# Kernel tuning notes

Measured on AMD Instinct MI355X. Metric: run time of the kernel, lower is better.

Reference implementation:

```python
import jax, jax.numpy as jnp
import numpy as np

EMBED_DIM = 512
NUM_HEADS = 8
TGT_LEN = 1024
BSZ = 16


def setup_inputs() -> dict:
    key = jax.random.key(0)
    ks = jax.random.split(key, 6)
    E = EMBED_DIM
    query = jax.random.normal(ks[0], (TGT_LEN, BSZ, E), jnp.float32)
    i_proj = jax.random.normal(ks[1], (3 * E,), jnp.float32)
    # xavier_uniform-ish scale for (3E, E)
    lim = (6.0 / (3 * E + E)) ** 0.5
    in_proj_weight = jax.random.uniform(ks[2], (3 * E, E), jnp.float32, -lim, lim)
    in_proj_bias = jnp.zeros((3 * E,), jnp.float32)
    lim2 = (6.0 / (2 * E)) ** 0.5
    out_w = jax.random.uniform(ks[3], (E, E), jnp.float32, -lim2, lim2)
    out_b = jnp.zeros((E,), jnp.float32)
    bias_k = jax.random.normal(ks[4], (1, 1, E), jnp.float32)
    bias_v = jax.random.normal(ks[5], (1, 1, E), jnp.float32)
    return dict(query=query, i_proj=i_proj, in_proj_weight=in_proj_weight,
                in_proj_bias=in_proj_bias, out_w=out_w, out_b=out_b,
                bias_k=bias_k, bias_v=bias_v)


def reference(query, i_proj, in_proj_weight, in_proj_bias, out_w, out_b, bias_k, bias_v):
    # qkv_same path: key = value = query (self-attention)
    T, B, E = query.shape
    H = NUM_HEADS
    hd = E // H
    scaling = hd ** -0.5
    # per-call weight mutation: every 3rd column replaced by i_proj
    w = in_proj_weight.at[:, ::3].set(i_proj[:, None])
    qkv = jnp.einsum('tbe,fe->tbf', query, w) + in_proj_bias  # (T, B, 3E)
    q, k, v = jnp.split(qkv, 3, axis=-1)
    q = q * scaling
    k = jnp.concatenate([k, jnp.broadcast_to(bias_k, (1, B, E))], axis=0)  # (T+1, B, E)
    v = jnp.concatenate([v, jnp.broadcast_to(bias_v, (1, B, E))], axis=0)
    S = k.shape[0]
    q = q.reshape(T, B * H, hd).transpose(1, 0, 2)  # (B*H, T, hd)
    k = k.reshape(S, B * H, hd).transpose(1, 0, 2)  # (B*H, S, hd)
    v = v.reshape(S, B * H, hd).transpose(1, 0, 2)
    aw = jnp.einsum('nth,nsh->nts', q, k)  # (B*H, T, S)
    # global min-max normalization over the entire score tensor (not softmax)
    mn = jnp.min(aw)
    mx = jnp.max(aw)
    aw = (aw - mn) / (mx - mn)
    attn = jnp.einsum('nts,nsh->nth', aw, v)  # (B*H, T, hd)
    attn = attn.transpose(1, 0, 2).reshape(T, B, E)
    attn = attn @ out_w.T + out_b  # out_proj
    aw_avg = aw.reshape(B, H, T, S).sum(axis=1) / H  # (B, T, S)
    wq, wk, wv = jnp.split(w, 3, axis=0)
    w_ret = jnp.stack([wq.T, wk.T, wv.T], axis=0)  # (3, E, E)
    return attn, aw_avg, w_ret
```

## Files before the change

### kernel.cpp

```cpp
#include <hip/hip_runtime.h>
#include <hip/hip_bf16.h>
#include <stdint.h>

typedef __bf16 bf16;
typedef __bf16 bf16x8 __attribute__((ext_vector_type(8)));
typedef __bf16 bf16x4 __attribute__((ext_vector_type(4)));
typedef float  f32x4  __attribute__((ext_vector_type(4)));

#define MFMA_BF16(a,b,c) __builtin_amdgcn_mfma_f32_16x16x32_bf16((a),(b),(c),0,0,0)

#define WS_QBF_IN  0L
#define WS_WBF     16777216L
#define WS_OUTWBF  18350080L
#define WS_Q       18874368L
#define WS_K       35651584L
#define WS_V       52428800L
#define WS_VT      69206016L
#define WS_AWLAST  85983232L
#define WS_VCS     86507520L
#define WS_MM      86540288L
#define WS_KT      86540544L
#define WS_KTV     103317760L

__device__ __forceinline__ void gload16(const void* g, void* l) {
  __builtin_amdgcn_global_load_lds((const __attribute__((address_space(1))) uint32_t*)g,
                                   (__attribute__((address_space(3))) uint32_t*)l, 16, 0, 0);
}
__device__ __forceinline__ unsigned ordf(float x) {
  unsigned b = __float_as_uint(x);
  return (b & 0x80000000u) ? ~b : (b | 0x80000000u);
}
__device__ __forceinline__ float deordf(unsigned u) {
  unsigned b = (u & 0x80000000u) ? (u ^ 0x80000000u) : ~u;
  return __uint_as_float(b);
}

__global__ __launch_bounds__(256) void cvt_query_kernel(const float* __restrict__ in,
                                                        bf16* __restrict__ out) {
  long i = (long)blockIdx.x * 256 + threadIdx.x;
  for (; i < 2097152L; i += (long)gridDim.x * 256) {
    float4 v = ((const float4*)in)[i];
    bf16x4 o; o[0] = (bf16)v.x; o[1] = (bf16)v.y; o[2] = (bf16)v.z; o[3] = (bf16)v.w;
    ((bf16x4*)out)[i] = o;
  }
}

__global__ __launch_bounds__(256) void prep_weights_kernel(
    const float* __restrict__ in_w, const float* __restrict__ i_proj,
    const float* __restrict__ out_w, bf16* __restrict__ w_bf,
    bf16* __restrict__ outw_bf, float* __restrict__ w_ret,
    unsigned* __restrict__ mm) {
  long idx = (long)blockIdx.x * 256 + threadIdx.x;
  if (idx == 0) { mm[0] = 0xFFFFFFFFu; mm[1] = 0u; }
  if (idx < 786432L) {
    int f = (int)(idx >> 9), e = (int)(idx & 511);
    float val = (e % 3 == 0) ? i_proj[f] : in_w[idx];
    w_bf[idx] = (bf16)val;
    w_ret[(long)(f >> 9) * 262144 + (long)e * 512 + (f & 511)] = val;
  } else if (idx < 1048576L) {
    long j = idx - 786432L;
    outw_bf[j] = (bf16)out_w[j];
  }
}

template <int MODE>
__global__ __launch_bounds__(256, 2) void gemm_kernel(
    const bf16* __restrict__ A, const bf16* __restrict__ B,
    const float* __restrict__ bias,
    bf16* __restrict__ q_out, bf16* __restrict__ k_out, bf16* __restrict__ v_out,
    float* __restrict__ outC) {
  const int K = 512;
  __shared__ __align__(16) bf16 aTile[128 * 32];
  __shared__ __align__(16) bf16 bTile[128 * 32];
  const int tid = threadIdx.x;
  const int lane = tid & 63, w = tid >> 6;
  const int l15 = lane & 15, l4 = lane >> 4;
  const long r0 = (long)blockIdx.y * 128;
  const long f0 = (long)blockIdx.x * 128;
  const int rm = (w >> 1) * 64, cn = (w & 1) * 64;
  const int srow = tid >> 2;
  const int scc = tid & 3;
  f32x4 acc[4][4] = {};

  for (int kk = 0; kk < K; kk += 32) {
#pragma unroll
    for (int i = 0; i < 2; ++i) {
      int row = srow + i * 64;
      int cc = scc ^ (row & 3);
      gload16(A + (r0 + row) * K + kk + cc * 8, (char*)aTile + (w * 64 + i * 256) * 16);
    }
#pragma unroll
    for (int i = 0; i < 2; ++i) {
      int row = srow + i * 64;
      int cc = scc ^ (row & 3);
      gload16(B + (f0 + row) * K + kk + cc * 8, (char*)bTile + (w * 64 + i * 256) * 16);
    }
    __syncthreads();
    bf16x8 af[4], bfr[4];
#pragma unroll
    for (int mi = 0; mi < 4; ++mi) {
      int r = rm + mi * 16 + l15;
      int c = l4 ^ (r & 3);
      af[mi] = *(const bf16x8*)((const char*)aTile + r * 64 + c * 16);
    }
#pragma unroll
    for (int ni = 0; ni < 4; ++ni) {
      int r = cn + ni * 16 + l15;
      int c = l4 ^ (r & 3);
      bfr[ni] = *(const bf16x8*)((const char*)bTile + r * 64 + c * 16);
    }
#pragma unroll
    for (int mi = 0; mi < 4; ++mi)
#pragma unroll
      for (int ni = 0; ni < 4; ++ni)
        acc[mi][ni] = MFMA_BF16(af[mi], bfr[ni], acc[mi][ni]);
    __syncthreads();
  }
#pragma unroll
  for (int mi = 0; mi < 4; ++mi)
#pragma unroll
    for (int ni = 0; ni < 4; ++ni)
#pragma unroll
      for (int r = 0; r < 4; ++r) {
        long row = r0 + rm + mi * 16 + l4 * 4 + r;
        int f = (int)f0 + cn + ni * 16 + l15;
        float val = acc[mi][ni][r] + bias[f];
        if (MODE == 0) {
          int t = (int)(row >> 4), b = (int)(row & 15);
          int which = f >> 9, hh = (f >> 6) & 7, d = f & 63;
          long off = ((long)(b * 8 + hh) * 1024 + t) * 64 + d;
          if (which == 0)      q_out[off] = (bf16)(val * 0.125f);
          else if (which == 1) k_out[off] = (bf16)val;
          else                 v_out[off] = (bf16)val;
        } else {
          outC[row * 512 + f] = val;
        }
      }
}

__global__ __launch_bounds__(256, 2) void awsum_gemm_kernel(
    const bf16* __restrict__ q_bf, const bf16* __restrict__ k_bf,
    float* __restrict__ aw_raw, unsigned* __restrict__ mm) {
  __shared__ __align__(16) bf16 aTile[128 * 32];
  __shared__ __align__(16) bf16 bTile[128 * 32];
  const int tid = threadIdx.x;
  const int lane = tid & 63, w = tid >> 6;
  const int l15 = lane & 15, l4 = lane >> 4;
  const int b = blockIdx.z;
  const int t0 = blockIdx.y * 128;
  const int s0 = blockIdx.x * 128;
  const int rm = (w >> 1) * 64, cn = (w & 1) * 64;
  const int srow = tid >> 2;
  const int scc = tid & 3;
  f32x4 acc[4][4] = {};
  f32x4 hsum[4][4] = {};
  float vmin = 1e30f, vmax = -1e30f;

  for (int kk = 0; kk < 512; kk += 32) {
    int h = kk >> 6, db = kk & 63;
#pragma unroll
    for (int i = 0; i < 2; ++i) {
      int row = srow + i * 64;
      int cc = scc ^ (row & 3);
      gload16(q_bf + ((long)(b * 8 + h) * 1024 + t0 + row) * 64 + db + cc * 8,
              (char*)aTile + (w * 64 + i * 256) * 16);
    }
#pragma unroll
    for (int i = 0; i < 2; ++i) {
      int row = srow + i * 64;
      int cc = scc ^ (row & 3);
      gload16(k_bf + ((long)(b * 8 + h) * 1024 + s0 + row) * 64 + db + cc * 8,
              (char*)bTile + (w * 64 + i * 256) * 16);
    }
    __syncthreads();
    bf16x8 af[4], bfr[4];
#pragma unroll
    for (int mi = 0; mi < 4; ++mi) {
      int r = rm + mi * 16 + l15;
      int c = l4 ^ (r & 3);
      af[mi] = *(const bf16x8*)((const char*)aTile + r * 64 + c * 16);
    }
#pragma unroll
    for (int ni = 0; ni < 4; ++ni) {
      int r = cn + ni * 16 + l15;
      int c = l4 ^ (r & 3);
      bfr[ni] = *(const bf16x8*)((const char*)bTile + r * 64 + c * 16);
    }
#pragma unroll
    for (int mi = 0; mi < 4; ++mi)
#pragma unroll
      for (int ni = 0; ni < 4; ++ni)
        acc[mi][ni] = MFMA_BF16(af[mi], bfr[ni], acc[mi][ni]);
    __syncthreads();
    if (kk & 32) {
#pragma unroll
      for (int mi = 0; mi < 4; ++mi)
#pragma unroll
        for (int ni = 0; ni < 4; ++ni) {
#pragma unroll
          for (int r = 0; r < 4; ++r) {
            float v = acc[mi][ni][r];
            vmin = fminf(vmin, v); vmax = fmaxf(vmax, v);
            hsum[mi][ni][r] += v;
          }
          acc[mi][ni] = (f32x4){0.f, 0.f, 0.f, 0.f};
        }
    }
  }
#pragma unroll
  for (int mi = 0; mi < 4; ++mi)
#pragma unroll
    for (int ni = 0; ni < 4; ++ni)
#pragma unroll
      for (int r = 0; r < 4; ++r) {
        int t = t0 + rm + mi * 16 + l4 * 4 + r;
        int s = s0 + cn + ni * 16 + l15;
        aw_raw[((long)b * 1024 + t) * 1025 + s] = hsum[mi][ni][r];
      }
#pragma unroll
  for (int off = 32; off; off >>= 1) {
    vmin = fminf(vmin, __shfl_xor(vmin, off));
    vmax = fmaxf(vmax, __shfl_xor(vmax, off));
  }
  if (lane == 0) { atomicMin(&mm[0], ordf(vmin)); atomicMax(&mm[1], ordf(vmax)); }
}

__global__ __launch_bounds__(256) void transpose_kv_kernel(
    const bf16* __restrict__ k_bf, const bf16* __restrict__ v_bf,
    bf16* __restrict__ kT, bf16* __restrict__ vT) {
  const bf16* src = blockIdx.z ? v_bf : k_bf;
  bf16* dst = blockIdx.z ? vT : kT;
  const int n = blockIdx.y;
  const long s0 = (long)blockIdx.x * 64;
  __shared__ __align__(16) bf16 tile[64][72];
  const int tid = threadIdx.x;
  const int row = tid >> 3, cc = tid & 7;
#pragma unroll
  for (int it = 0; it < 2; ++it) {
    int r = row + it * 32;
    bf16x8 vv = *(const bf16x8*)(src + ((long)n * 1024 + s0 + r) * 64 + cc * 8);
    *(bf16x8*)&tile[r][cc * 8] = vv;
  }
  __syncthreads();
#pragma unroll
  for (int it = 0; it < 2; ++it) {
    int d = row + it * 32;
    bf16x8 ov;
#pragma unroll
    for (int j = 0; j < 8; ++j) ov[j] = tile[cc * 8 + j][d];
    *(bf16x8*)(dst + ((long)n * 64 + d) * 1024 + s0 + cc * 8) = ov;
  }
}

__global__ __launch_bounds__(256) void vcolsum_kernel(const bf16* __restrict__ v_bf,
                                                      const float* __restrict__ bias_v,
                                                      float* __restrict__ vcs) {
  const int n = blockIdx.x, h = n & 7;
  const int d = threadIdx.x & 63, g = threadIdx.x >> 6;
  float acc = 0.f;
  const bf16* base = v_bf + (long)n * 65536 + d;
  for (int s = g * 256; s < g * 256 + 256; ++s) acc += (float)base[(long)s * 64];
  __shared__ float red[4][64];
  red[g][d] = acc;
  __syncthreads();
  if (g == 0) vcs[n * 64 + d] = red[0][d] + red[1][d] + red[2][d] + red[3][d] + bias_v[h * 64 + d];
}

__global__ __launch_bounds__(256) void ktv_kernel(const bf16* __restrict__ kT,
                                                  const bf16* __restrict__ vT,
                                                  bf16* __restrict__ ktvT) {
  const int n = blockIdx.x;
  const int tid = threadIdx.x;
  const int lane = tid & 63, w = tid >> 6;
  const int l15 = lane & 15, l4 = lane >> 4;
  const int wr = w >> 1, wc = w & 1;
  f32x4 acc[2][2] = {};
  const bf16* kbase = kT + (long)n * 65536;
  const bf16* vbase = vT + (long)n * 65536;
  for (int s0 = 0; s0 < 1024; s0 += 32) {
    bf16x8 af[2], bfr[2];
#pragma unroll
    for (int mi = 0; mi < 2; ++mi)
      af[mi] = *(const bf16x8*)(kbase + (long)(wr * 32 + mi * 16 + l15) * 1024 + s0 + l4 * 8);
#pragma unroll
    for (int ni = 0; ni < 2; ++ni)
      bfr[ni] = *(const bf16x8*)(vbase + (long)(wc * 32 + ni * 16 + l15) * 1024 + s0 + l4 * 8);
#pragma unroll
    for (int mi = 0; mi < 2; ++mi)
#pragma unroll
      for (int ni = 0; ni < 2; ++ni)
        acc[mi][ni] = MFMA_BF16(af[mi], bfr[ni], acc[mi][ni]);
  }
#pragma unroll
  for (int mi = 0; mi < 2; ++mi)
#pragma unroll
    for (int ni = 0; ni < 2; ++ni)
#pragma unroll
      for (int r = 0; r < 4; ++r) {
        int d = wr * 32 + mi * 16 + l4 * 4 + r;
        int dp = wc * 32 + ni * 16 + l15;
        ktvT[(long)n * 4096 + dp * 64 + d] = (bf16)acc[mi][ni][r];
      }
}

__global__ __launch_bounds__(256) void qattn_kernel(
    const bf16* __restrict__ q_bf, const bf16* __restrict__ ktvT,
    const float* __restrict__ aw_last, const float* __restrict__ vcs,
    const float* __restrict__ bias_v, const unsigned* __restrict__ mm,
    bf16* __restrict__ A2) {
  const int tid = threadIdx.x;
  const int lane = tid & 63, w = tid >> 6;
  const int l15 = lane & 15, l4 = lane >> 4;
  const int t0 = blockIdx.x * 64;
  const int h = blockIdx.y * 4 + w;
  const int b = blockIdx.z;
  const long n = (long)b * 8 + h;
  f32x4 acc[4][4] = {};
  const bf16* qbase = q_bf + (n * 1024 + t0) * 64;
  const bf16* kbase = ktvT + (long)n * 4096;
#pragma unroll
  for (int kk = 0; kk < 64; kk += 32) {
    bf16x8 af[4], bfr[4];
#pragma unroll
    for (int mi = 0; mi < 4; ++mi)
      af[mi] = *(const bf16x8*)(qbase + (mi * 16 + l15) * 64 + kk + l4 * 8);
#pragma unroll
    for (int ni = 0; ni < 4; ++ni)
      bfr[ni] = *(const bf16x8*)(kbase + (ni * 16 + l15) * 64 + kk + l4 * 8);
#pragma unroll
    for (int mi = 0; mi < 4; ++mi)
#pragma unroll
      for (int ni = 0; ni < 4; ++ni)
        acc[mi][ni] = MFMA_BF16(af[mi], bfr[ni], acc[mi][ni]);
  }
  float mn = deordf(mm[0]), mx = deordf(mm[1]);
  float a = 1.f / (mx - mn), c = -mn * a;
#pragma unroll
  for (int mi = 0; mi < 4; ++mi)
#pragma unroll
    for (int r = 0; r < 4; ++r) {
      int t = t0 + mi * 16 + l4 * 4 + r;
      float alast = a * aw_last[n * 1024 + t];
#pragma unroll
      for (int ni = 0; ni < 4; ++ni) {
        int dp = ni * 16 + l15;
        float val = a * acc[mi][ni][r] + alast * bias_v[h * 64 + dp] + c * vcs[n * 64 + dp];
        A2[((long)t * 16 + b) * 512 + h * 64 + dp] = (bf16)val;
      }
    }
}

__global__ __launch_bounds__(256) void bias_col_kernel(const bf16* __restrict__ q_bf,
                                                       const float* __restrict__ bias_k,
                                                       float* __restrict__ aw_last,
                                                       unsigned* __restrict__ mm) {
  const int n = blockIdx.y, h = n & 7;
  const int t = blockIdx.x * 256 + threadIdx.x;
  float acc = 0.f;
  const bf16* qrow = q_bf + ((long)n * 1024 + t) * 64;
#pragma unroll
  for (int j = 0; j < 8; ++j) {
    bf16x8 qv = *(const bf16x8*)(qrow + j * 8);
#pragma unroll
    for (int e = 0; e < 8; ++e) acc += (float)qv[e] * bias_k[h * 64 + j * 8 + e];
  }
  aw_last[(long)n * 1024 + t] = acc;
  float vmin = acc, vmax = acc;
#pragma unroll
  for (int off = 32; off; off >>= 1) {
    vmin = fminf(vmin, __shfl_xor(vmin, off));
    vmax = fmaxf(vmax, __shfl_xor(vmax, off));
  }
  if ((threadIdx.x & 63) == 0) { atomicMin(&mm[0], ordf(vmin)); atomicMax(&mm[1], ordf(vmax)); }
}

__global__ __launch_bounds__(256) void rescale_kernel(float* __restrict__ aw_out,
                                                      const float* __restrict__ aw_last,
                                                      const unsigned* __restrict__ mm) {
  long idx = (long)blockIdx.x * 256 + threadIdx.x;
  float mn = deordf(mm[0]), mx = deordf(mm[1]);
  float a = 1.f / (mx - mn), c = -mn * a;
  int s = (int)(idx % 1025);
  long bt = idx / 1025;
  float v;
  if (s < 1024) {
    v = aw_out[idx];
  } else {
    int b = (int)(bt >> 10), t = (int)(bt & 1023);
    v = 0.f;
#pragma unroll
    for (int h = 0; h < 8; ++h) v += aw_last[(long)(b * 8 + h) * 1024 + t];
  }
  aw_out[idx] = fmaf(a, v * 0.125f, c);
}

extern "C" void kernel_launch(void* const* d_in, const int* in_sizes, int n_in,
                              void* d_out, int out_size, void* d_ws, size_t ws_size,
                              hipStream_t stream) {
  const float* query  = (const float*)d_in[0];
  const float* i_proj = (const float*)d_in[1];
  const float* in_w   = (const float*)d_in[2];
  const float* in_b   = (const float*)d_in[3];
  const float* out_w  = (const float*)d_in[4];
  const float* out_b  = (const float*)d_in[5];
  const float* bias_k = (const float*)d_in[6];
  const float* bias_v = (const float*)d_in[7];
  float* out = (float*)d_out;

  char* ws = (char*)d_ws;
  bf16* qbf_in = (bf16*)(ws + WS_QBF_IN);
  bf16* w_bf   = (bf16*)(ws + WS_WBF);
  bf16* outwbf = (bf16*)(ws + WS_OUTWBF);
  bf16* q_bf   = (bf16*)(ws + WS_Q);
  bf16* k_bf   = (bf16*)(ws + WS_K);
  bf16* v_bf   = (bf16*)(ws + WS_V);
  bf16* vT     = (bf16*)(ws + WS_VT);
  bf16* kT     = (bf16*)(ws + WS_KT);
  bf16* ktvT   = (bf16*)(ws + WS_KTV);
  float* aw_last = (float*)(ws + WS_AWLAST);
  float* vcs     = (float*)(ws + WS_VCS);
  unsigned* mm   = (unsigned*)(ws + WS_MM);
  bf16* A2 = qbf_in;

  float* out_attn  = out;
  float* out_awavg = out + 8388608L;
  float* out_wret  = out + 25182208L;

  cvt_query_kernel<<<2048, 256, 0, stream>>>(query, qbf_in);
  prep_weights_kernel<<<4096, 256, 0, stream>>>(in_w, i_proj, out_w, w_bf, outwbf, out_wret, mm);
  gemm_kernel<0><<<dim3(12, 128), 256, 0, stream>>>(qbf_in, w_bf, in_b, q_bf, k_bf, v_bf, nullptr);
  transpose_kv_kernel<<<dim3(16, 128, 2), 256, 0, stream>>>(k_bf, v_bf, kT, vT);
  vcolsum_kernel<<<128, 256, 0, stream>>>(v_bf, bias_v, vcs);
  bias_col_kernel<<<dim3(4, 128), 256, 0, stream>>>(q_bf, bias_k, aw_last, mm);
  awsum_gemm_kernel<<<dim3(8, 8, 16), 256, 0, stream>>>(q_bf, k_bf, out_awavg, mm);
  ktv_kernel<<<128, 256, 0, stream>>>(kT, vT, ktvT);
  rescale_kernel<<<65600, 256, 0, stream>>>(out_awavg, aw_last, mm);
  qattn_kernel<<<dim3(16, 2, 16), 256, 0, stream>>>(q_bf, ktvT, aw_last, vcs, bias_v, mm, A2);
  gemm_kernel<1><<<dim3(4, 128), 256, 0, stream>>>(A2, outwbf, out_b, nullptr, nullptr, nullptr, out_attn);
}
```

Baseline: 322.5 us.

## Double-buffer awsum GEMM, store raw scores in bf16, remap blocks per XCD

The awsum score GEMM gets double-buffered LDS tiles so the next K-slice load overlaps MFMA work. Per-head min/max now comes from differences against a snapshot of the running accumulator, so the separate head-sum accumulator goes away. Raw summed scores go to a compact bf16 scratch buffer (reusing the V workspace) that the rescale kernel reads, instead of an fp32 in-place pass over the output. Blocks are remapped so each XCD handles contiguous batches, and vcolsum now reads the transposed V with vector loads. The bf16 intermediate loses precision in the averaged weights, and taking the difference of cumulative sums adds rounding to the min/max.

Measured after the change: 318.2 us. Within noise of the previous version (-1.3%).

```diff
diff --git a/kernel.cpp b/kernel.cpp
--- a/kernel.cpp
+++ b/kernel.cpp
@@ -138,74 +138,85 @@
       }
 }
 
+#define AWS_STAGE(kk, buf)                                                            \
+  do {                                                                                \
+    int h_ = (kk) >> 1, db_ = ((kk) & 1) * 32;                                        \
+    _Pragma("unroll")                                                                 \
+    for (int i_ = 0; i_ < 2; ++i_) {                                                  \
+      int row_ = srow + i_ * 64;                                                      \
+      int cc_ = scc ^ (row_ & 3);                                                     \
+      gload16(q_bf + ((long)(b * 8 + h_) * 1024 + t0 + row_) * 64 + db_ + cc_ * 8,    \
+              (char*)aT[buf] + (w * 64 + i_ * 256) * 16);                             \
+      gload16(k_bf + ((long)(b * 8 + h_) * 1024 + s0 + row_) * 64 + db_ + cc_ * 8,    \
+              (char*)bT[buf] + (w * 64 + i_ * 256) * 16);                             \
+    }                                                                                 \
+  } while (0)
+
+#define AWS_COMPUTE(buf)                                                              \
+  do {                                                                                \
+    bf16x8 af[4], bfr[4];                                                             \
+    _Pragma("unroll")                                                                 \
+    for (int mi_ = 0; mi_ < 4; ++mi_) {                                               \
+      int r_ = rm + mi_ * 16 + l15;                                                   \
+      int c_ = l4 ^ (r_ & 3);                                                         \
+      af[mi_] = *(const bf16x8*)((const char*)aT[buf] + r_ * 64 + c_ * 16);           \
+    }                                                                                 \
+    _Pragma("unroll")                                                                 \
+    for (int ni_ = 0; ni_ < 4; ++ni_) {                                               \
+      int r_ = cn + ni_ * 16 + l15;                                                   \
+      int c_ = l4 ^ (r_ & 3);                                                         \
+      bfr[ni_] = *(const bf16x8*)((const char*)bT[buf] + r_ * 64 + c_ * 16);          \
+    }                                                                                 \
+    _Pragma("unroll")                                                                 \
+    for (int mi_ = 0; mi_ < 4; ++mi_)                                                 \
+      _Pragma("unroll")                                                               \
+      for (int ni_ = 0; ni_ < 4; ++ni_)                                               \
+        acc[mi_][ni_] = MFMA_BF16(af[mi_], bfr[ni_], acc[mi_][ni_]);                  \
+  } while (0)
+
 __global__ __launch_bounds__(256, 2) void awsum_gemm_kernel(
     const bf16* __restrict__ q_bf, const bf16* __restrict__ k_bf,
-    float* __restrict__ aw_raw, unsigned* __restrict__ mm) {
-  __shared__ __align__(16) bf16 aTile[128 * 32];
-  __shared__ __align__(16) bf16 bTile[128 * 32];
+    bf16* __restrict__ aw_raw, unsigned* __restrict__ mm) {
+  __shared__ __align__(16) bf16 aT[2][128 * 32];
+  __shared__ __align__(16) bf16 bT[2][128 * 32];
   const int tid = threadIdx.x;
   const int lane = tid & 63, w = tid >> 6;
   const int l15 = lane & 15, l4 = lane >> 4;
-  const int b = blockIdx.z;
-  const int t0 = blockIdx.y * 128;
-  const int s0 = blockIdx.x * 128;
+  const int bid = blockIdx.x;
+  const int xcd = bid & 7, slot = bid >> 3;
+  const int b = xcd * 2 + (slot >> 6);
+  const int rest = slot & 63;
+  const int t0 = (rest >> 3) * 128;
+  const int s0 = (rest & 7) * 128;
   const int rm = (w >> 1) * 64, cn = (w & 1) * 64;
   const int srow = tid >> 2;
   const int scc = tid & 3;
+
   f32x4 acc[4][4] = {};
-  f32x4 hsum[4][4] = {};
+  f32x4 snap[4][4] = {};
   float vmin = 1e30f, vmax = -1e30f;
 
-  for (int kk = 0; kk < 512; kk += 32) {
-    int h = kk >> 6, db = kk & 63;
-#pragma unroll
-    for (int i = 0; i < 2; ++i) {
-      int row = srow + i * 64;
-      int cc = scc ^ (row & 3);
-      gload16(q_bf + ((long)(b * 8 + h) * 1024 + t0 + row) * 64 + db + cc * 8,
-              (char*)aTile + (w * 64 + i * 256) * 16);
-    }
-#pragma unroll
-    for (int i = 0; i < 2; ++i) {
-      int row = srow + i * 64;
-      int cc = scc ^ (row & 3);
-      gload16(k_bf + ((long)(b * 8 + h) * 1024 + s0 + row) * 64 + db + cc * 8,
-              (char*)bTile + (w * 64 + i * 256) * 16);
-    }
+  AWS_STAGE(0, 0);
+  __syncthreads();
+  for (int h = 0; h < 8; ++h) {
+    AWS_STAGE(2 * h + 1, 1);
+    AWS_COMPUTE(0);
     __syncthreads();
-    bf16x8 af[4], bfr[4];
-#pragma unroll
-    for (int mi = 0; mi < 4; ++mi) {
-      int r = rm + mi * 16 + l15;
-      int c = l4 ^ (r & 3);
-      af[mi] = *(const bf16x8*)((const char*)aTile + r * 64 + c * 16);
-    }
-#pragma unroll
-    for (int ni = 0; ni < 4; ++ni) {
-      int r = cn + ni * 16 + l15;
-      int c = l4 ^ (r & 3);
-      bfr[ni] = *(const bf16x8*)((const char*)bTile + r * 64 + c * 16);
-    }
+    if (h < 7) AWS_STAGE(2 * h + 2, 0);
+    AWS_COMPUTE(1);
 #pragma unroll
     for (int mi = 0; mi < 4; ++mi)
 #pragma unroll
-      for (int ni = 0; ni < 4; ++ni)
-        acc[mi][ni] = MFMA_BF16(af[mi], bfr[ni], acc[mi][ni]);
+      for (int ni = 0; ni < 4; ++ni) {
+        f32x4 d = acc[mi][ni] - snap[mi][ni];
+#pragma unroll
+        for (int r = 0; r < 4; ++r) {
+          vmin = fminf(vmin, d[r]);
+          vmax = fmaxf(vmax, d[r]);
+        }
+        snap[mi][ni] = acc[mi][ni];
+      }
     __syncthreads();
-    if (kk & 32) {
-#pragma unroll
-      for (int mi = 0; mi < 4; ++mi)
-#pragma unroll
-        for (int ni = 0; ni < 4; ++ni) {
-#pragma unroll
-          for (int r = 0; r < 4; ++r) {
-            float v = acc[mi][ni][r];
-            vmin = fminf(vmin, v); vmax = fmaxf(vmax, v);
-            hsum[mi][ni][r] += v;
-          }
-          acc[mi][ni] = (f32x4){0.f, 0.f, 0.f, 0.f};
-        }
-    }
   }
 #pragma unroll
   for (int mi = 0; mi < 4; ++mi)
@@ -215,7 +226,7 @@
       for (int r = 0; r < 4; ++r) {
         int t = t0 + rm + mi * 16 + l4 * 4 + r;
         int s = s0 + cn + ni * 16 + l15;
-        aw_raw[((long)b * 1024 + t) * 1025 + s] = hsum[mi][ni][r];
+        aw_raw[((long)b * 1024 + t) * 1024 + s] = (bf16)acc[mi][ni][r];
       }
 #pragma unroll
   for (int off = 32; off; off >>= 1) {
@@ -252,18 +263,25 @@
   }
 }
 
-__global__ __launch_bounds__(256) void vcolsum_kernel(const bf16* __restrict__ v_bf,
+__global__ __launch_bounds__(256) void vcolsum_kernel(const bf16* __restrict__ vT,
                                                       const float* __restrict__ bias_v,
                                                       float* __restrict__ vcs) {
   const int n = blockIdx.x, h = n & 7;
-  const int d = threadIdx.x & 63, g = threadIdx.x >> 6;
+  const int d = threadIdx.x >> 2, q = threadIdx.x & 3;
   float acc = 0.f;
-  const bf16* base = v_bf + (long)n * 65536 + d;
-  for (int s = g * 256; s < g * 256 + 256; ++s) acc += (float)base[(long)s * 64];
-  __shared__ float red[4][64];
-  red[g][d] = acc;
+  const bf16* row = vT + (long)n * 65536 + (long)d * 1024 + q * 256;
+#pragma unroll 4
+  for (int j = 0; j < 32; ++j) {
+    bf16x8 v = *(const bf16x8*)(row + j * 8);
+#pragma unroll
+    for (int e = 0; e < 8; ++e) acc += (float)v[e];
+  }
+  __shared__ float red[256];
+  red[threadIdx.x] = acc;
   __syncthreads();
-  if (g == 0) vcs[n * 64 + d] = red[0][d] + red[1][d] + red[2][d] + red[3][d] + bias_v[h * 64 + d];
+  if (q == 0)
+    vcs[n * 64 + d] = red[d * 4] + red[d * 4 + 1] + red[d * 4 + 2] + red[d * 4 + 3] +
+                      bias_v[h * 64 + d];
 }
 
 __global__ __launch_bounds__(256) void ktv_kernel(const bf16* __restrict__ kT,
@@ -374,7 +392,8 @@
   if ((threadIdx.x & 63) == 0) { atomicMin(&mm[0], ordf(vmin)); atomicMax(&mm[1], ordf(vmax)); }
 }
 
-__global__ __launch_bounds__(256) void rescale_kernel(float* __restrict__ aw_out,
+__global__ __launch_bounds__(256) void rescale_kernel(const bf16* __restrict__ aw_raw,
+                                                      float* __restrict__ aw_out,
                                                       const float* __restrict__ aw_last,
                                                       const unsigned* __restrict__ mm) {
   long idx = (long)blockIdx.x * 256 + threadIdx.x;
@@ -384,7 +403,7 @@
   long bt = idx / 1025;
   float v;
   if (s < 1024) {
-    v = aw_out[idx];
+    v = (float)aw_raw[bt * 1024 + s];
   } else {
     int b = (int)(bt >> 10), t = (int)(bt & 1023);
     v = 0.f;
@@ -417,6 +436,7 @@
   bf16* vT     = (bf16*)(ws + WS_VT);
   bf16* kT     = (bf16*)(ws + WS_KT);
   bf16* ktvT   = (bf16*)(ws + WS_KTV);
+  bf16* aw_raw = (bf16*)(ws + WS_V);
   float* aw_last = (float*)(ws + WS_AWLAST);
   float* vcs     = (float*)(ws + WS_VCS);
   unsigned* mm   = (unsigned*)(ws + WS_MM);
@@ -430,11 +450,11 @@
   prep_weights_kernel<<<4096, 256, 0, stream>>>(in_w, i_proj, out_w, w_bf, outwbf, out_wret, mm);
   gemm_kernel<0><<<dim3(12, 128), 256, 0, stream>>>(qbf_in, w_bf, in_b, q_bf, k_bf, v_bf, nullptr);
   transpose_kv_kernel<<<dim3(16, 128, 2), 256, 0, stream>>>(k_bf, v_bf, kT, vT);
-  vcolsum_kernel<<<128, 256, 0, stream>>>(v_bf, bias_v, vcs);
+  vcolsum_kernel<<<128, 256, 0, stream>>>(vT, bias_v, vcs);
   bias_col_kernel<<<dim3(4, 128), 256, 0, stream>>>(q_bf, bias_k, aw_last, mm);
-  awsum_gemm_kernel<<<dim3(8, 8, 16), 256, 0, stream>>>(q_bf, k_bf, out_awavg, mm);
   ktv_kernel<<<128, 256, 0, stream>>>(kT, vT, ktvT);
-  rescale_kernel<<<65600, 256, 0, stream>>>(out_awavg, aw_last, mm);
+  awsum_gemm_kernel<<<1024, 256, 0, stream>>>(q_bf, k_bf, aw_raw, mm);
+  rescale_kernel<<<65600, 256, 0, stream>>>(aw_raw, out_awavg, aw_last, mm);
   qattn_kernel<<<dim3(16, 2, 16), 256, 0, stream>>>(q_bf, ktvT, aw_last, vcs, bias_v, mm, A2);
   gemm_kernel<1><<<dim3(4, 128), 256, 0, stream>>>(A2, outwbf, out_b, nullptr, nullptr, nullptr, out_attn);
 }
```
